# Optimization experiments

Measured on AMD Instinct MI355X. Metric: run time of the kernel, lower is better.

Reference implementation:

```python
import jax, jax.numpy as jnp
import numpy as np

N_FFT = 1024
HOP = 256
WIN = N_FFT  # win_length = n_fft in VocosISTFTHead
PAD = (WIN - HOP) // 2  # 384, 'same' padding trim
CLAMP_MAX = 100.0


def _hann_periodic(n):
    # matches torch.hann_window(n, periodic=True)
    return 0.5 * (1.0 - jnp.cos(2.0 * jnp.pi * jnp.arange(n, dtype=jnp.float32) / n))


def setup_inputs() -> dict:
    key = jax.random.key(0)
    k1, k2, k3 = jax.random.split(key, 3)
    B, T, H = 16, 2048, 512
    hidden_states = jax.random.normal(k1, (B, T, H), dtype=jnp.float32)
    # out_proj: Linear(hidden_dim, n_fft+2); scaled so exp(magnitude) stays sane
    W = jax.random.normal(k2, (N_FFT + 2, H), dtype=jnp.float32) * 0.02
    b = jax.random.normal(k3, (N_FFT + 2,), dtype=jnp.float32) * 0.02
    window = _hann_periodic(WIN)
    return {"hidden_states": hidden_states, "W": W, "b": b, "window": window}


def reference(hidden_states, W, b, window):
    B, T, _ = hidden_states.shape
    # linear projection -> [B, T, n_fft+2] -> transpose -> [B, n_fft+2, T]
    spec = (hidden_states @ W.T + b).transpose(0, 2, 1)
    half = (N_FFT + 2) // 2  # n_fft//2 + 1 = 513 freq bins
    magnitude = jnp.minimum(jnp.exp(spec[:, :half]), CLAMP_MAX)
    phase = spec[:, half:]
    coeffs = magnitude * (jnp.cos(phase) + 1j * jnp.sin(phase))  # [B, F, T] complex
    # inverse rfft along freq axis, norm='backward' (default) -> [B, n_fft, T]
    frames = jnp.fft.irfft(coeffs, n=N_FFT, axis=1)
    frames = frames * window[None, :, None]
    L = (T - 1) * HOP + WIN
    idx = (jnp.arange(T)[:, None] * HOP + jnp.arange(WIN)[None, :]).reshape(-1)
    frames_flat = frames.transpose(0, 2, 1).reshape(B, -1)
    audio = jnp.zeros((B, L), frames.dtype).at[:, idx].add(frames_flat)
    # NOLA normalization: overlap-added squared window
    wsq = jnp.broadcast_to(window ** 2, (T, WIN)).reshape(-1)
    norm = jnp.zeros((L,), window.dtype).at[idx].add(wsq)
    return audio[:, PAD:-PAD] / norm[PAD:-PAD]
```

## Files before the change

kernel.cpp:

```cpp
#include <hip/hip_runtime.h>
#include <hip/hip_fp16.h>
#include <math.h>
#include <stdint.h>


#define FRAMES  32768
#define TWO_PI  6.283185307179586f

typedef unsigned short ushort_t;
typedef __attribute__((ext_vector_type(8))) _Float16 f16x8;
typedef __attribute__((ext_vector_type(4))) float f32x4;

#define GLDS(gp, lp) __builtin_amdgcn_global_load_lds( \
    (const __attribute__((address_space(1))) void*)(gp), \
    (__attribute__((address_space(3))) void*)(lp), 16, 0, 0)

__device__ __forceinline__ float2 f2(float x, float y){ return make_float2(x,y); }
__device__ __forceinline__ float2 cadd(float2 a, float2 b){ return f2(a.x+b.x, a.y+b.y); }
__device__ __forceinline__ float2 csub(float2 a, float2 b){ return f2(a.x-b.x, a.y-b.y); }
__device__ __forceinline__ float2 cmul(float2 a, float2 b){ return f2(a.x*b.x - a.y*b.y, a.x*b.y + a.y*b.x); }

__device__ __forceinline__ uint32_t pack2h(float a, float b) {
  const ushort_t ha = __half_as_ushort(__float2half_rn(a));
  const ushort_t hb = __half_as_ushort(__float2half_rn(b));
  return (uint32_t)ha | ((uint32_t)hb << 16);
}

__global__ __launch_bounds__(256) void convert_AB(
    const float* __restrict__ hs, const float* __restrict__ Wm,
    const float* __restrict__ bias, ushort_t* __restrict__ Af,
    ushort_t* __restrict__ Whi, __half* __restrict__ coeffs)
{
  const int bid = blockIdx.x;
  const int t = threadIdx.x;
  if (bid < 2048) {
    const int r = t >> 4, c = t & 15;
    const int m = bid * 16 + r;
    const float* src = hs + (size_t)m * 512 + c * 32;
    const float* wm  = Wm + (size_t)512  * 512 + c * 32;
    const float* wp  = Wm + (size_t)1025 * 512 + c * 32;

    float v[32];
    #pragma unroll
    for (int i = 0; i < 8; ++i) *(float4*)&v[i*4] = *(const float4*)(src + i*4);

    float dm = 0.f, dp = 0.f;
    #pragma unroll
    for (int i = 0; i < 8; ++i) {
      const float4 a  = *(const float4*)&v[i*4];
      const float4 m4 = *(const float4*)(wm + i*4);
      const float4 p4 = *(const float4*)(wp + i*4);
      dm = fmaf(a.x,m4.x, fmaf(a.y,m4.y, fmaf(a.z,m4.z, fmaf(a.w,m4.w, dm))));
      dp = fmaf(a.x,p4.x, fmaf(a.y,p4.y, fmaf(a.z,p4.z, fmaf(a.w,p4.w, dp))));
    }

    uint32_t hu[16];
    #pragma unroll
    for (int i = 0; i < 16; ++i) hu[i] = pack2h(v[2*i], v[2*i+1]);
    ushort_t* dh = Af + (size_t)m * 512 + c * 32;
    #pragma unroll
    for (int q = 0; q < 4; ++q)
      *(uint4*)(dh + q*8) = make_uint4(hu[4*q], hu[4*q+1], hu[4*q+2], hu[4*q+3]);

    #pragma unroll
    for (int off = 8; off; off >>= 1) {
      dm += __shfl_xor(dm, off, 16);
      dp += __shfl_xor(dp, off, 16);
    }
    if (c == 0) {
      const float sm = dm + bias[512], sp = dp + bias[1025];
      const float mag = fminf(__expf(sm), 100.0f);
      coeffs[(size_t)m * 1024 + 1] = __float2half_rn(mag * __cosf(sp));
    }
  } else {
    const int gid = (bid - 2048) * 256 + t;
    const int sd = gid & 3;
    const int r  = (gid >> 2) & 255;
    const int kt = (gid >> 10) & 15;
    const int yb = gid >> 14;
    const int srow = (r < 128) ? (yb*128 + r) : (513 + yb*128 + (r - 128));
    const float* src = Wm + (size_t)srow * 512 + kt*32 + sd*8;
    const float4 a = *(const float4*)src;
    const float4 b = *(const float4*)(src + 4);
    const uint4 o = make_uint4(pack2h(a.x,a.y), pack2h(a.z,a.w),
                               pack2h(b.x,b.y), pack2h(b.z,b.w));
    *(uint4*)(Whi + (size_t)gid * 8) = o;
  }
}

__global__ __launch_bounds__(512, 2) void gemm_mfma(
    const ushort_t* __restrict__ Af, const ushort_t* __restrict__ Whi,
    const float* __restrict__ bias, __half* __restrict__ coeffs)
{
  __shared__ ushort_t Ab[24576];

  const int tid = threadIdx.x;
  const int w = tid >> 6, l = tid & 63;
  const int wr = w >> 2, wc = w & 3;
  const int lc = l & 15, kg = l >> 4;

  const int bid = blockIdx.x;
  const int swz = (bid & 7) * 64 + (bid >> 3);
  const int mb = swz >> 2, yb = swz & 3;

  uint32_t pa_off[2], lofs[2];
  #pragma unroll
  for (int ch = 0; ch < 2; ++ch) {
    const int g = ch*512 + tid;
    const int r = g >> 2, sd = g & 3;
    lofs[ch] = r*32 + sd*8;
    const int sl = sd ^ ((r >> 1) & 3);
    pa_off[ch] = (uint32_t)(mb*256 + r)*512 + sl*8;
  }
  uint32_t pb_off[4];
  #pragma unroll
  for (int cf = 0; cf < 4; ++cf) {
    const int rB = ((cf < 2) ? 0 : 128) + wc*32 + (cf & 1)*16 + lc;
    pb_off[cf] = (uint32_t)yb*131072u + rB*32 + kg*8;
  }

  f32x4 acc[8][4];
  #pragma unroll
  for (int rf = 0; rf < 8; ++rf)
    #pragma unroll
    for (int cf = 0; cf < 4; ++cf)
      #pragma unroll
      for (int q = 0; q < 4; ++q) acc[rf][cf][q] = 0.f;

  const int asl = (kg ^ ((lc >> 1) & 3)) * 8;

  f16x8 p[4], q[4];

#define WAITV2 asm volatile("s_waitcnt vmcnt(2) lgkmcnt(0)" ::: "memory")
#define WAITV0 asm volatile("s_waitcnt vmcnt(0) lgkmcnt(0)" ::: "memory")
#define SB     __builtin_amdgcn_s_barrier()
#define SCH0   __builtin_amdgcn_sched_barrier(0)

#define DSREAD(DST, BASE, RF0) do {                                      \
    _Pragma("unroll")                                                    \
    for (int r4 = 0; r4 < 4; ++r4) {                                     \
      const int rr = wr*128 + ((RF0) + r4)*16 + lc;                      \
      DST[r4] = *(const f16x8*)(&Ab[(BASE) + rr*32 + asl]);              \
    }                                                                    \
  } while (0)

#define MFMA16(FA, RF0, RB) do {                                         \
    __builtin_amdgcn_s_setprio(1);                                       \
    _Pragma("unroll")                                                    \
    for (int r4 = 0; r4 < 4; ++r4)                                       \
      _Pragma("unroll")                                                  \
      for (int cf = 0; cf < 4; ++cf)                                     \
        acc[(RF0)+r4][cf] = __builtin_amdgcn_mfma_f32_16x16x32_f16(      \
            FA[r4], RB[cf], acc[(RF0)+r4][cf], 0, 0, 0);                 \
    __builtin_amdgcn_s_setprio(0);                                       \
  } while (0)

#define ITER(KT, RBC, RBN, LAST) do {                                    \
    if (LAST) { WAITV0; } else { WAITV2; }                               \
    SB;                                                                  \
               \
    DSREAD(q, aR, 4);                                                    \
    if ((KT) < 14) GLDS(Af + pa_off[0] + ((KT)+2)*32, &Ab[aW + lofs[0]]);\
    if ((KT) < 15) {                                                     \
      RBN[0] = *(const f16x8*)(Whi + pb_off[0] + ((KT)+1)*8192);         \
      RBN[1] = *(const f16x8*)(Whi + pb_off[1] + ((KT)+1)*8192);         \
    }                                                                    \
    SCH0;                                                                \
    MFMA16(p, 0, RBC);                                                   \
    SB;                                                                  \
               \
    if ((KT) < 15) DSREAD(p, aN, 0);                                     \
    if ((KT) < 14) GLDS(Af + pa_off[1] + ((KT)+2)*32, &Ab[aW + lofs[1]]);\
    if ((KT) < 15) {                                                     \
      RBN[2] = *(const f16x8*)(Whi + pb_off[2] + ((KT)+1)*8192);         \
      RBN[3] = *(const f16x8*)(Whi + pb_off[3] + ((KT)+1)*8192);         \
    }                                                                    \
    SCH0;                                                                \
    MFMA16(q, 4, RBC);                                                   \
    { const unsigned t_ = aR; aR = aN; aN = aW; aW = t_; }               \
  } while (0)

  f16x8 rb0[4], rb1[4];
  GLDS(Af + pa_off[0], &Ab[lofs[0]]);
  GLDS(Af + pa_off[1], &Ab[lofs[1]]);
  GLDS(Af + pa_off[0] + 32, &Ab[8192 + lofs[0]]);
  GLDS(Af + pa_off[1] + 32, &Ab[8192 + lofs[1]]);
  SCH0;
  #pragma unroll
  for (int j = 0; j < 4; ++j) rb0[j] = *(const f16x8*)(Whi + pb_off[j]);
  SCH0;
  asm volatile("s_waitcnt vmcnt(6)" ::: "memory");
  SB;
  unsigned aR = 0, aN = 8192, aW = 16384;
  DSREAD(p, aR, 0);

  for (int k2 = 0; k2 < 8; ++k2) {
    ITER(2*k2,     rb0, rb1, false);
    ITER(2*k2 + 1, rb1, rb0, k2 == 7);
  }
#undef ITER
#undef DSREAD
#undef MFMA16

  #pragma unroll
  for (int j = 0; j < 2; ++j) {
    const int pcol = yb*128 + wc*32 + j*16 + lc;
    const float bm = bias[pcol], bp = bias[513 + pcol];
    #pragma unroll
    for (int rf = 0; rf < 8; ++rf) {
      const int rbase = mb*256 + wr*128 + rf*16 + kg*4;
      #pragma unroll
      for (int qi = 0; qi < 4; ++qi) {
        const float sm = acc[rf][j][qi]   + bm;
        const float sp = acc[rf][2+j][qi] + bp;
        const float mag = fminf(__expf(sm), 100.0f);
        const float aa = mag * __cosf(sp);
        const float bb = mag * __sinf(sp);
        __half* row = coeffs + (size_t)(rbase + qi) * 1024;
        if (pcol == 0) row[0] = __float2half_rn(aa);
        else *(__half2*)(row + 2*pcol) = __float22half2_rn(make_float2(aa, bb));
      }
    }
  }
}

#define PIDX(s) ((s) + ((s) >> 3))

template<int NS>
__device__ __forceinline__ void stage_fft(const float2* in, float2* out, int l)
{
  float2 v[8];
  #pragma unroll
  for (int r = 0; r < 8; ++r) v[r] = in[PIDX(l + 64*r)];
  if (NS > 1) {
    const float ang = TWO_PI * (float)(l & (NS-1)) / (float)(NS * 8);
    float sn, cs; __sincosf(ang, &sn, &cs);
    const float2 wb = f2(cs, sn);
    float2 cur = wb;
    #pragma unroll
    for (int r = 1; r < 8; ++r) { v[r] = cmul(v[r], cur); cur = cmul(cur, wb); }
  }
  const float2 e0=v[0], e1=v[2], e2=v[4], e3=v[6];
  const float2 o0=v[1], o1=v[3], o2=v[5], o3=v[7];
  float2 a = cadd(e0,e2), b = csub(e0,e2), c = cadd(e1,e3), d = csub(e1,e3);
  const float2 E0 = cadd(a,c), E2 = csub(a,c);
  const float2 E1 = f2(b.x - d.y, b.y + d.x), E3 = f2(b.x + d.y, b.y - d.x);
  a = cadd(o0,o2); b = csub(o0,o2); c = cadd(o1,o3); d = csub(o1,o3);
  const float2 O0 = cadd(a,c), O2 = csub(a,c);
  const float2 O1 = f2(b.x - d.y, b.y + d.x), O3 = f2(b.x + d.y, b.y - d.x);
  const float r2 = 0.70710678118654752f;
  const float2 t0 = O0;
  const float2 t1 = f2(r2*(O1.x - O1.y),  r2*(O1.x + O1.y));
  const float2 t2 = f2(-O2.y, O2.x);
  const float2 t3 = f2(-r2*(O3.x + O3.y), r2*(O3.x - O3.y));
  float2 X[8];
  X[0]=cadd(E0,t0); X[4]=csub(E0,t0);
  X[1]=cadd(E1,t1); X[5]=csub(E1,t1);
  X[2]=cadd(E2,t2); X[6]=csub(E2,t2);
  X[3]=cadd(E3,t3); X[7]=csub(E3,t3);
  const int idxD = (l / NS) * (NS * 8) + (l & (NS-1));
  #pragma unroll
  for (int q = 0; q < 8; ++q) out[PIDX(idxD + q*NS)] = X[q];
}

__global__ __launch_bounds__(256) void fft_win(
    const __half* coeffs, __half* frames, const float* __restrict__ window)
{
  __shared__ float2 bA[4][576];
  __shared__ float2 bB[4][576];
  const int tid = threadIdx.x;
  const int w = tid >> 6, l = tid & 63;
  const size_t f = (size_t)blockIdx.x * 4 + w;
  const __half2* crow = (const __half2*)(coeffs + f * 1024);

  const float sc = 1.0f / 1024.0f;
  #pragma unroll
  for (int j = 0; j < 4; ++j) {
    const int k = 1 + l + 64*j;
    const float2 Ck = __half22float2(crow[k]);
    const float2 Cq = __half22float2(crow[512-k]);
    float sn, cs; __sincosf(TWO_PI * (1.0f/1024.0f) * (float)k, &sn, &cs);
    const float Ex = sc*(Ck.x + Cq.x), Ey = sc*(Ck.y - Cq.y);
    const float Dx = Ck.x - Cq.x,      Dy = Ck.y + Cq.y;
    const float Ox = sc*(cs*Dx - sn*Dy), Oy = sc*(cs*Dy + sn*Dx);
    bA[w][PIDX(k)]     = f2(Ex - Oy, Ey + Ox);
    bA[w][PIDX(512-k)] = f2(Ex + Oy, Ox - Ey);
  }
  if (l == 0) {
    const float2 dn = __half22float2(crow[0]);
    bA[w][PIDX(0)] = f2(sc*(dn.x + dn.y), sc*(dn.x - dn.y));
  }
  __syncthreads();
  stage_fft<1 >(bA[w], bB[w], l);
  __syncthreads();
  stage_fft<8 >(bB[w], bA[w], l);
  __syncthreads();
  stage_fft<64>(bA[w], bB[w], l);
  __syncthreads();

  __half2* frow = (__half2*)(frames + f * 1024);
  #pragma unroll
  for (int j = 0; j < 8; ++j) {
    const int m = l + 64*j;
    const float2 z  = bB[w][PIDX(m)];
    const float2 wv = *(const float2*)(window + 2*m);
    frow[m] = __float22half2_rn(make_float2(z.x * wv.x, z.y * wv.y));
  }
}

__global__ __launch_bounds__(256) void gather_out(
    const __half* __restrict__ frames, const float* __restrict__ window,
    float* __restrict__ out)
{
  const int idx = blockIdx.x * 256 + threadIdx.x;
  const int b  = idx >> 19;
  const int jj = idx & 524287;
  const int s  = jj + 384;
  int tlo = (s - 768) >> 8; if (tlo < 0) tlo = 0;
  int thi = s >> 8;         if (thi > 2047) thi = 2047;
  float acc = 0.f, nrm = 0.f;
  for (int t = tlo; t <= thi; ++t) {
    const int n = s - (t << 8);
    const float wv = window[n];
    nrm = fmaf(wv, wv, nrm);
    acc += __half2float(frames[(size_t)(b * 2048 + t) * 1024 + n]);
  }
  out[idx] = acc / nrm;
}

extern "C" void kernel_launch(void* const* d_in, const int* in_sizes, int n_in,
                              void* d_out, int out_size, void* d_ws, size_t ws_size,
                              hipStream_t stream)
{
  const float* hs     = (const float*)d_in[0];
  const float* Wm     = (const float*)d_in[1];
  const float* bias   = (const float*)d_in[2];
  const float* window = (const float*)d_in[3];

  char* base = (char*)d_ws;
  ushort_t* Af     = (ushort_t*)base;
  ushort_t* Whi    = (ushort_t*)(base + 33554432);
  __half*   frames = (__half*)base;
  __half*   coeffs = (__half*)(base + 67108864);

  convert_AB<<<2304, 256, 0, stream>>>(hs, Wm, bias, Af, Whi, coeffs);
  gemm_mfma<<<512,  512, 0, stream>>>(Af, Whi, bias, coeffs);
  fft_win<<<FRAMES / 4, 256, 0, stream>>>(coeffs, frames, window);
  gather_out<<<8388608 / 256, 256, 0, stream>>>(frames, window, (float*)d_out);
}
```

Before: 150.6 us.

## Double GEMM waves per block and halve rows computed per wave

Launches the MFMA GEMM with 1024 threads (16 waves) instead of 512, with each wave covering 64 rows instead of 128 of the same 256x256 tile. Accumulators and A fragments per wave are halved, and the A-tile global-to-LDS copy drops to one load per thread. The pipeline wait counts are re-tuned to match. The aim is more latency hiding through extra waves and lower register pressure. In exchange, each wave still loads its full set of B fragments, so B register traffic doubles, and the aggressive launch bounds may force register limits or spills.

```diff
diff --git a/kernel.cpp b/kernel.cpp
--- a/kernel.cpp
+++ b/kernel.cpp
@@ -88,7 +88,7 @@
   }
 }
 
-__global__ __launch_bounds__(512, 2) void gemm_mfma(
+__global__ __launch_bounds__(1024, 4) void gemm_mfma(
     const ushort_t* __restrict__ Af, const ushort_t* __restrict__ Whi,
     const float* __restrict__ bias, __half* __restrict__ coeffs)
 {
@@ -103,14 +103,12 @@
   const int swz = (bid & 7) * 64 + (bid >> 3);
   const int mb = swz >> 2, yb = swz & 3;
 
-  uint32_t pa_off[2], lofs[2];
-  #pragma unroll
-  for (int ch = 0; ch < 2; ++ch) {
-    const int g = ch*512 + tid;
-    const int r = g >> 2, sd = g & 3;
-    lofs[ch] = r*32 + sd*8;
+  uint32_t pa_off, lofs;
+  {
+    const int r = tid >> 2, sd = tid & 3;
+    lofs = r*32 + sd*8;
     const int sl = sd ^ ((r >> 1) & 3);
-    pa_off[ch] = (uint32_t)(mb*256 + r)*512 + sl*8;
+    pa_off = (uint32_t)(mb*256 + r)*512 + sl*8;
   }
   uint32_t pb_off[4];
   #pragma unroll
@@ -119,9 +117,9 @@
     pb_off[cf] = (uint32_t)yb*131072u + rB*32 + kg*8;
   }
 
-  f32x4 acc[8][4];
-  #pragma unroll
-  for (int rf = 0; rf < 8; ++rf)
+  f32x4 acc[4][4];
+  #pragma unroll
+  for (int rf = 0; rf < 4; ++rf)
     #pragma unroll
     for (int cf = 0; cf < 4; ++cf)
       #pragma unroll
@@ -129,25 +127,27 @@
 
   const int asl = (kg ^ ((lc >> 1) & 3)) * 8;
 
-  f16x8 p[4], q[4];
-
-#define WAITV2 asm volatile("s_waitcnt vmcnt(2) lgkmcnt(0)" ::: "memory")
+  f16x8 p[2], q[2];
+
+#define WAITV1 asm volatile("s_waitcnt vmcnt(1) lgkmcnt(0)" ::: "memory")
 #define WAITV0 asm volatile("s_waitcnt vmcnt(0) lgkmcnt(0)" ::: "memory")
+#define WAITP5 asm volatile("s_waitcnt vmcnt(5)" ::: "memory")
+#define WAITP4 asm volatile("s_waitcnt vmcnt(4)" ::: "memory")
 #define SB     __builtin_amdgcn_s_barrier()
 #define SCH0   __builtin_amdgcn_sched_barrier(0)
 
 #define DSREAD(DST, BASE, RF0) do {                                      \
     _Pragma("unroll")                                                    \
-    for (int r4 = 0; r4 < 4; ++r4) {                                     \
-      const int rr = wr*128 + ((RF0) + r4)*16 + lc;                      \
+    for (int r4 = 0; r4 < 2; ++r4) {                                     \
+      const int rr = wr*64 + ((RF0) + r4)*16 + lc;                       \
       DST[r4] = *(const f16x8*)(&Ab[(BASE) + rr*32 + asl]);              \
     }                                                                    \
   } while (0)
 
-#define MFMA16(FA, RF0, RB) do {                                         \
+#define MFMA8(FA, RF0, RB) do {                                          \
     __builtin_amdgcn_s_setprio(1);                                       \
     _Pragma("unroll")                                                    \
-    for (int r4 = 0; r4 < 4; ++r4)                                       \
+    for (int r4 = 0; r4 < 2; ++r4)                                       \
       _Pragma("unroll")                                                  \
       for (int cf = 0; cf < 4; ++cf)                                     \
         acc[(RF0)+r4][cf] = __builtin_amdgcn_mfma_f32_16x16x32_f16(      \
@@ -156,40 +156,39 @@
   } while (0)
 
 #define ITER(KT, RBC, RBN, LAST) do {                                    \
-    if (LAST) { WAITV0; } else { WAITV2; }                               \
+    if (LAST) { WAITV0; } else { WAITV1; }                               \
     SB;                                                                  \
-               \
-    DSREAD(q, aR, 4);                                                    \
-    if ((KT) < 14) GLDS(Af + pa_off[0] + ((KT)+2)*32, &Ab[aW + lofs[0]]);\
+           \
+    DSREAD(q, aR, 2);                                                    \
     if ((KT) < 15) {                                                     \
-      RBN[0] = *(const f16x8*)(Whi + pb_off[0] + ((KT)+1)*8192);         \
-      RBN[1] = *(const f16x8*)(Whi + pb_off[1] + ((KT)+1)*8192);         \
+      _Pragma("unroll")                                                  \
+      for (int j = 0; j < 4; ++j)                                        \
+        RBN[j] = *(const f16x8*)(Whi + pb_off[j] + ((KT)+1)*8192);       \
+    }                                                                    \
+    if ((KT) < 14) GLDS(Af + pa_off + ((KT)+2)*32, &Ab[aW + lofs]);      \
+    SCH0;                                                                \
+    MFMA8(p, 0, RBC);                                                    \
+    SB;                                                                  \
+           \
+    if ((KT) < 15) {                                                     \
+      if ((KT) < 14) { WAITP5; } else { WAITP4; }                        \
+      SCH0;                                                              \
+      DSREAD(p, aN, 0);                                                  \
     }                                                                    \
     SCH0;                                                                \
-    MFMA16(p, 0, RBC);                                                   \
-    SB;                                                                  \
-               \
-    if ((KT) < 15) DSREAD(p, aN, 0);                                     \
-    if ((KT) < 14) GLDS(Af + pa_off[1] + ((KT)+2)*32, &Ab[aW + lofs[1]]);\
-    if ((KT) < 15) {                                                     \
-      RBN[2] = *(const f16x8*)(Whi + pb_off[2] + ((KT)+1)*8192);         \
-      RBN[3] = *(const f16x8*)(Whi + pb_off[3] + ((KT)+1)*8192);         \
-    }                                                                    \
-    SCH0;                                                                \
-    MFMA16(q, 4, RBC);                                                   \
+    MFMA8(q, 2, RBC);                                                    \
     { const unsigned t_ = aR; aR = aN; aN = aW; aW = t_; }               \
   } while (0)
 
   f16x8 rb0[4], rb1[4];
-  GLDS(Af + pa_off[0], &Ab[lofs[0]]);
-  GLDS(Af + pa_off[1], &Ab[lofs[1]]);
-  GLDS(Af + pa_off[0] + 32, &Ab[8192 + lofs[0]]);
-  GLDS(Af + pa_off[1] + 32, &Ab[8192 + lofs[1]]);
+  GLDS(Af + pa_off, &Ab[lofs]);
   SCH0;
   #pragma unroll
   for (int j = 0; j < 4; ++j) rb0[j] = *(const f16x8*)(Whi + pb_off[j]);
   SCH0;
-  asm volatile("s_waitcnt vmcnt(6)" ::: "memory");
+  GLDS(Af + pa_off + 32, &Ab[8192 + lofs]);
+  SCH0;
+  asm volatile("s_waitcnt vmcnt(5)" ::: "memory");
   SB;
   unsigned aR = 0, aN = 8192, aW = 16384;
   DSREAD(p, aR, 0);
@@ -200,15 +199,15 @@
   }
 #undef ITER
 #undef DSREAD
-#undef MFMA16
+#undef MFMA8
 
   #pragma unroll
   for (int j = 0; j < 2; ++j) {
     const int pcol = yb*128 + wc*32 + j*16 + lc;
     const float bm = bias[pcol], bp = bias[513 + pcol];
     #pragma unroll
-    for (int rf = 0; rf < 8; ++rf) {
-      const int rbase = mb*256 + wr*128 + rf*16 + kg*4;
+    for (int rf = 0; rf < 4; ++rf) {
+      const int rbase = mb*256 + wr*64 + rf*16 + kg*4;
       #pragma unroll
       for (int qi = 0; qi < 4; ++qi) {
         const float sm = acc[rf][j][qi]   + bm;
@@ -344,7 +343,7 @@
   __half*   coeffs = (__half*)(base + 67108864);
 
   convert_AB<<<2304, 256, 0, stream>>>(hs, Wm, bias, Af, Whi, coeffs);
-  gemm_mfma<<<512,  512, 0, stream>>>(Af, Whi, bias, coeffs);
+  gemm_mfma<<<512, 1024, 0, stream>>>(Af, Whi, bias, coeffs);
   fft_win<<<FRAMES / 4, 256, 0, stream>>>(coeffs, frames, window);
   gather_out<<<8388608 / 256, 256, 0, stream>>>(frames, window, (float*)d_out);
 }
```

Measured after the change: 176.1 us. 16.9% more time.
